# Kernel optimization log

Measured on AMD Instinct MI355X. Metric: run time of the kernel, lower is better.

The kernel has to match this reference:

```python
import jax, jax.numpy as jnp
import numpy as np

C_IN = 128
C_HID = 32
N_HEADS = 4
INF = 1000000000.0


def setup_inputs() -> dict:
    key = jax.random.key(0)
    ks = jax.random.split(key, 12)
    B, I, J = 1, 256, 256
    hc = N_HEADS * C_HID
    s = 0.02
    return {
        "x": jax.random.normal(ks[0], (B, I, J, C_IN), dtype=jnp.float32),
        "mask": jnp.ones((B, I, J), dtype=jnp.float32),
        "ln_w": jnp.ones((C_IN,), dtype=jnp.float32),
        "ln_b": jnp.zeros((C_IN,), dtype=jnp.float32),
        "w_tri": jax.random.normal(ks[1], (C_IN, N_HEADS), dtype=jnp.float32) * s,
        "wq": jax.random.normal(ks[2], (C_IN, hc), dtype=jnp.float32) * s,
        "wk": jax.random.normal(ks[3], (C_IN, hc), dtype=jnp.float32) * s,
        "wv": jax.random.normal(ks[4], (C_IN, hc), dtype=jnp.float32) * s,
        "wg": jax.random.normal(ks[5], (C_IN, hc), dtype=jnp.float32) * s,
        "bg": jnp.ones((hc,), dtype=jnp.float32),
        "wo": jax.random.normal(ks[6], (hc, C_IN), dtype=jnp.float32) * s,
        "bo": jnp.zeros((C_IN,), dtype=jnp.float32),
    }


def _layer_norm(x, w, b, eps=1e-5):
    mu = jnp.mean(x, axis=-1, keepdims=True)
    var = jnp.var(x, axis=-1, keepdims=True)
    return (x - mu) * jax.lax.rsqrt(var + eps) * w + b


def _triangle_attention(x, mask, ln_w, ln_b, w_tri, wq, wk, wv, wg, bg, wo, bo):
    # starting=True: no transpose. x: [B, I, J, C]
    B, I, J, C = x.shape
    x = _layer_norm(x, ln_w, ln_b)
    # mask_bias: [B, I, 1, 1, J]
    mask_bias = (INF * (mask - 1.0))[..., :, None, None, :]
    # triangle_bias: linear(x) -> [B, I, J, H], permute (2,0,1) -> [B, H, I, J], unsqueeze -> [B, 1, H, I, J]
    tri = jnp.einsum("bijc,ch->bhij", x, w_tri)[:, None]  # [B, 1, H, I, J]
    # q/k/v: [B, I, H, J, Ch]
    def proj(w):
        return jnp.einsum("bijc,c(" + "" + ")->bijc", x, w) if False else (
            (x @ w).reshape(B, I, J, N_HEADS, C_HID).transpose(0, 1, 3, 2, 4))
    q = proj(wq) * (C_HID ** -0.5)
    k = proj(wk)
    v = proj(wv)
    # scores: [B, I, H, J, J]; biases broadcast over H (mask_bias) / I (tri over b,1 dim matches i? no)
    scores = jnp.einsum("bihqc,bihkc->bihqk", q, k)
    scores = scores + mask_bias + tri  # tri [B,1,H,I,J] broadcasts: i-dim aligns with query? matches torch broadcast [B,I,H,J,J]+[B,1,H,J,J]... wait tri is [B,1,H,I,J] with I==J so it broadcasts over the batch-of-rows dim
    a = jax.nn.softmax(scores, axis=-1)
    o = jnp.einsum("bihqk,bihkc->bihqc", a, v)  # [B, I, H, J, Ch]
    o = o.transpose(0, 1, 3, 2, 4).reshape(B, I, J, N_HEADS * C_HID)
    g = jax.nn.sigmoid(x @ wg + bg)
    o = o * g
    return o @ wo + bo  # [B, I, J, C]


def reference(x, mask, ln_w, ln_b, w_tri, wq, wk, wv, wg, bg, wo, bo):
    return _triangle_attention(x, mask, ln_w, ln_b, w_tri, wq, wk, wv, wg, bg, wo, bo)
```

## Files before the change

### kernel.cpp

```cpp
#include <hip/hip_runtime.h>


typedef __attribute__((ext_vector_type(4))) float f32x4;
typedef __attribute__((ext_vector_type(8))) short bf16x8;
#define MFMA16(a, b, c) __builtin_amdgcn_mfma_f32_16x16x32_bf16(a, b, c, 0, 0, 0)
#define LOG2E 1.4426950408889634f

__device__ __forceinline__ float bf2f(unsigned int u16) {
    return __uint_as_float(u16 << 16);
}
__device__ __forceinline__ unsigned int f2bf(float f) {
    unsigned int u = __float_as_uint(f);
    return (u + 0x7fffu + ((u >> 16) & 1u)) >> 16;
}
__device__ __forceinline__ unsigned int pack2(float a, float b) {
    return f2bf(a) | (f2bf(b) << 16);
}
__device__ __forceinline__ unsigned int cvt_pk_bf16(float lo, float hi) {
    unsigned int r;
    asm("v_cvt_pk_bf16_f32 %0, %1, %2" : "=v"(r) : "v"(lo), "v"(hi));
    return r;
}

__global__ __launch_bounds__(128) void k_prep(
    const float* __restrict__ wq, const float* __restrict__ wk,
    const float* __restrict__ wv, const float* __restrict__ wg,
    const float* __restrict__ wo, unsigned short* __restrict__ wT)
{
    const int mat = blockIdx.x, k0 = blockIdx.y * 16, t = threadIdx.x;
    const float* W = (mat == 0) ? wq : (mat == 1) ? wk : (mat == 2) ? wv
                     : (mat == 3) ? wg : wo;
    unsigned short* T = wT + mat * 16384;
    float col[16];
    #pragma unroll
    for (int kk = 0; kk < 16; ++kk) col[kk] = W[(k0 + kk) * 128 + t];
    unsigned int pk[8];
    #pragma unroll
    for (int u = 0; u < 8; ++u) pk[u] = pack2(col[2 * u], col[2 * u + 1]);
    *(uint4*)(T + t * 128 + k0)     = make_uint4(pk[0], pk[1], pk[2], pk[3]);
    *(uint4*)(T + t * 128 + k0 + 8) = make_uint4(pk[4], pk[5], pk[6], pk[7]);
}

__global__ __launch_bounds__(256, 2) void k_lnproj(
    const float* __restrict__ x, const float* __restrict__ ln_w,
    const float* __restrict__ ln_b, const float* __restrict__ w_tri,
    const unsigned short* __restrict__ wT, const float* __restrict__ bg,
    unsigned short* __restrict__ qb, unsigned short* __restrict__ kb,
    unsigned short* __restrict__ vtb, unsigned short* __restrict__ gb,
    float* __restrict__ triT)
{
    __shared__ unsigned short sA[128 * 136];
    __shared__ unsigned short sB[128 * 136];
    __shared__ unsigned short sWt[16 * 136];

    const int t = threadIdx.x, w = t >> 6, lane = t & 63;
    const int l15 = lane & 15, g = lane >> 4;
    const int rowBase = blockIdx.x * 128;

    if (t < 128) {
        const float4 wv = ((const float4*)w_tri)[t];
        sWt[0 * 136 + t] = (unsigned short)f2bf(wv.x);
        sWt[1 * 136 + t] = (unsigned short)f2bf(wv.y);
        sWt[2 * 136 + t] = (unsigned short)f2bf(wv.z);
        sWt[3 * 136 + t] = (unsigned short)f2bf(wv.w);
    } else {
        #pragma unroll
        for (int u = 0; u < 13; ++u) {
            const int idx = (t - 128) + 128 * u;
            if (idx < 12 * 136) sWt[4 * 136 + idx] = 0;
        }
    }

    {
        const int r = t >> 1, half = t & 1;
        const float* xr = x + (size_t)(rowBase + r) * 128 + half * 64;
        float v[64];
        float s1 = 0.0f, s2 = 0.0f;
        #pragma unroll
        for (int u = 0; u < 16; ++u) {
            const float4 q4 = ((const float4*)xr)[u];
            v[4*u] = q4.x; v[4*u+1] = q4.y; v[4*u+2] = q4.z; v[4*u+3] = q4.w;
            s1 += q4.x + q4.y + q4.z + q4.w;
            s2 += q4.x*q4.x + q4.y*q4.y + q4.z*q4.z + q4.w*q4.w;
        }
        s1 += __shfl_xor(s1, 1);
        s2 += __shfl_xor(s2, 1);
        const float mu = s1 * (1.0f / 128.0f);
        const float rs = rsqrtf(s2 * (1.0f / 128.0f) - mu * mu + 1e-5f);
        const float4* lw = (const float4*)(ln_w + half * 64);
        const float4* lb = (const float4*)(ln_b + half * 64);
        #pragma unroll
        for (int u = 0; u < 16; ++u) {
            const float4 w4 = lw[u], b4 = lb[u];
            v[4*u]   = (v[4*u]   - mu) * rs * w4.x + b4.x;
            v[4*u+1] = (v[4*u+1] - mu) * rs * w4.y + b4.y;
            v[4*u+2] = (v[4*u+2] - mu) * rs * w4.z + b4.z;
            v[4*u+3] = (v[4*u+3] - mu) * rs * w4.w + b4.w;
        }
        #pragma unroll
        for (int u = 0; u < 8; ++u) {
            uint4 pk;
            pk.x = pack2(v[8*u],   v[8*u+1]);
            pk.y = pack2(v[8*u+2], v[8*u+3]);
            pk.z = pack2(v[8*u+4], v[8*u+5]);
            pk.w = pack2(v[8*u+6], v[8*u+7]);
            *(uint4*)&sA[r * 136 + half * 64 + u * 8] = pk;
        }
    }
    __syncthreads();

    bf16x8 af[2][4];
    #pragma unroll
    for (int m = 0; m < 2; ++m)
        #pragma unroll
        for (int ks = 0; ks < 4; ++ks)
            af[m][ks] = *(const bf16x8*)&sA[(w * 32 + m * 16 + l15) * 136 + ks * 32 + g * 8];

    #pragma unroll
    for (int m = 0; m < 2; ++m) {
        f32x4 tc = (f32x4){0.f, 0.f, 0.f, 0.f};
        #pragma unroll
        for (int ks = 0; ks < 4; ++ks) {
            const bf16x8 bfw = *(const bf16x8*)&sWt[l15 * 136 + ks * 32 + g * 8];
            tc = MFMA16(af[m][ks], bfw, tc);
        }
        if (l15 < 4) {
            #pragma unroll
            for (int reg = 0; reg < 4; ++reg) {
                const int gr = rowBase + w * 32 + m * 16 + 4 * g + reg;
                triT[l15 * 65536 + gr] = tc[reg] * LOG2E;
            }
        }
    }

    const int r2 = t >> 1, half2 = t & 1;
    for (int mat = 0; mat < 4; ++mat) {
        {
            const unsigned short* Wm = wT + mat * 16384 + r2 * 128 + half2 * 64;
            #pragma unroll
            for (int u = 0; u < 8; ++u)
                *(uint4*)&sB[r2 * 136 + half2 * 64 + u * 8] = *(const uint4*)(Wm + u * 8);
        }
        __syncthreads();

        f32x4 acc[2][8];
        #pragma unroll
        for (int m = 0; m < 2; ++m)
            #pragma unroll
            for (int n = 0; n < 8; ++n) acc[m][n] = (f32x4){0.f, 0.f, 0.f, 0.f};
        #pragma unroll
        for (int n = 0; n < 8; ++n)
            #pragma unroll
            for (int ks = 0; ks < 4; ++ks) {
                const bf16x8 bf = *(const bf16x8*)&sB[(n * 16 + l15) * 136 + ks * 32 + g * 8];
                acc[0][n] = MFMA16(af[0][ks], bf, acc[0][n]);
                acc[1][n] = MFMA16(af[1][ks], bf, acc[1][n]);
            }
        __syncthreads();

        float bgv[8];
        if (mat == 3) {
            #pragma unroll
            for (int n = 0; n < 8; ++n) bgv[n] = bg[n * 16 + l15];
        }
        const float scl = (mat == 0) ? 0.25503486245f : 1.0f;
        #pragma unroll
        for (int m = 0; m < 2; ++m)
            #pragma unroll
            for (int n = 0; n < 8; ++n) {
                float vv[4];
                #pragma unroll
                for (int reg = 0; reg < 4; ++reg) {
                    float z = acc[m][n][reg];
                    if (mat == 3) z = 1.0f / (1.0f + __expf(-(z + bgv[n])));
                    else z *= scl;
                    vv[reg] = z;
                }
                const unsigned int a01 = cvt_pk_bf16(vv[0], vv[1]);
                const unsigned int a23 = cvt_pk_bf16(vv[2], vv[3]);
                const int qr = w * 32 + m * 16 + g * 4;
                const int col = n * 16 + l15;
                sB[qr * 136 + col]       = (unsigned short)a01;
                sB[(qr + 1) * 136 + col] = (unsigned short)(a01 >> 16);
                sB[(qr + 2) * 136 + col] = (unsigned short)a23;
                sB[(qr + 3) * 136 + col] = (unsigned short)(a23 >> 16);
            }
        __syncthreads();

        const int row = rowBase + r2;
        if (mat < 2) {
            unsigned short* dst = (mat == 0) ? qb : kb;
            const int i = row >> 8, j = row & 255;
            #pragma unroll
            for (int u = 0; u < 8; ++u) {
                const int c0 = half2 * 64 + u * 8;
                const int hh = c0 >> 5, ch = c0 & 31;
                *(uint4*)(dst + (((size_t)(i * 4 + hh)) * 256 + j) * 32 + ch) =
                    *(const uint4*)&sB[r2 * 136 + c0];
            }
        } else if (mat == 2) {
            const int c = t & 127, jh = t >> 7;
            const int i = rowBase >> 8;
            const int j0 = (rowBase & 255) + jh * 64;
            unsigned short buf[64];
            #pragma unroll
            for (int u = 0; u < 64; ++u) buf[u] = sB[(jh * 64 + u) * 136 + c];
            unsigned short* dst = vtb + ((size_t)(i * 128 + c)) * 256 + j0;
            #pragma unroll
            for (int u = 0; u < 8; ++u)
                *(uint4*)(dst + u * 8) = *(uint4*)&buf[u * 8];
        } else {
            #pragma unroll
            for (int u = 0; u < 8; ++u) {
                const int c0 = half2 * 64 + u * 8;
                *(uint4*)(gb + (size_t)row * 128 + c0) = *(const uint4*)&sB[r2 * 136 + c0];
            }
        }
        __syncthreads();
    }
}

__global__ __launch_bounds__(256, 3) void k_attn6(
    const unsigned short* __restrict__ qb, const unsigned short* __restrict__ kb,
    const unsigned short* __restrict__ vtb, const float* __restrict__ mask,
    const float* __restrict__ triT, const unsigned short* __restrict__ gb,
    unsigned short* __restrict__ ob)
{
    __shared__ unsigned short sK[256 * 32];
    __shared__ unsigned short sVt[32 * 260];
    __shared__ unsigned short sP[4][64 * 36];
    __shared__ float sM[256];

    const int i = blockIdx.x, h = blockIdx.y, t = threadIdx.x;
    const int w = t >> 6, lane = t & 63, l15 = lane & 15, g = lane >> 4;
    const size_t base = (size_t)(i * 4 + h) * 8192;

    {
        const uint4* ks = (const uint4*)(kb + base + t * 32);
        char* kdst = (char*)sK + t * 64;
        const int kswz = (t & 3) << 4;
        #pragma unroll
        for (int u = 0; u < 4; ++u)
            *(uint4*)(kdst + ((u * 16) ^ kswz)) = ks[u];

        const int ch = t >> 3, seg = t & 7;
        const uint4* vs = (const uint4*)(vtb + base + (size_t)ch * 256 + seg * 32);
        unsigned short* vdst = &sVt[ch * 260 + seg * 32];
        #pragma unroll
        for (int u = 0; u < 4; ++u)
            *(uint4*)(vdst + u * 8) = vs[u];

        sM[t] = (LOG2E * 1.0e9f) * (mask[i * 256 + t] - 1.0f);
    }

    const int q0 = w * 64;
    bf16x8 qf[4];
    #pragma unroll
    for (int m = 0; m < 4; ++m)
        qf[m] = *(const bf16x8*)(qb + base + (size_t)(q0 + m * 16 + l15) * 32 + g * 8);

    bf16x8 ones;
    #pragma unroll
    for (int u = 0; u < 8; ++u) ones[u] = (short)0x3F80;

    __syncthreads();

    f32x4 acc[4][2], accL[4];
    #pragma unroll
    for (int m = 0; m < 4; ++m) {
        acc[m][0] = (f32x4){0.f, 0.f, 0.f, 0.f};
        acc[m][1] = (f32x4){0.f, 0.f, 0.f, 0.f};
        accL[m]   = (f32x4){0.f, 0.f, 0.f, 0.f};
    }

    unsigned short* sPw = &sP[w][0];
    const float* triQ = triT + h * 65536;
    const f32x4 zero = (f32x4){0.f, 0.f, 0.f, 0.f};

    #pragma unroll
    for (int kt = 0; kt < 4; ++kt) {
        const int kv0 = kt * 64;
        #pragma unroll
        for (int hh = 0; hh < 2; ++hh) {
            const int kvh = kv0 + hh * 32;

            bf16x8 kf[2];
            #pragma unroll
            for (int n2 = 0; n2 < 2; ++n2) {
                const int row = kvh + n2 * 16 + l15;
                kf[n2] = *(const bf16x8*)((const char*)sK + row * 64 +
                                          ((g * 16) ^ ((row & 3) << 4)));
            }
            float4 mk[2];
            #pragma unroll
            for (int n2 = 0; n2 < 2; ++n2)
                mk[n2] = *(const float4*)&sM[kvh + n2 * 16 + g * 4];

            float4 tvb[2][2];
            #pragma unroll
            for (int n2 = 0; n2 < 2; ++n2)
                tvb[0][n2] = *(const float4*)
                    (triQ + (q0 + l15) * 256 + kvh + n2 * 16 + g * 4);

            #pragma unroll
            for (int m = 0; m < 4; ++m) {
                f32x4 p[2];
                #pragma unroll
                for (int n2 = 0; n2 < 2; ++n2)
                    p[n2] = MFMA16(kf[n2], qf[m], zero);
                if (m < 3) {
                    #pragma unroll
                    for (int n2 = 0; n2 < 2; ++n2)
                        tvb[(m + 1) & 1][n2] = *(const float4*)
                            (triQ + (q0 + (m + 1) * 16 + l15) * 256 + kvh + n2 * 16 + g * 4);
                }
                #pragma unroll
                for (int n2 = 0; n2 < 2; ++n2) {
                    const float4 tv = tvb[m & 1][n2];
                    p[n2][0] = exp2f(p[n2][0] + mk[n2].x + tv.x);
                    p[n2][1] = exp2f(p[n2][1] + mk[n2].y + tv.y);
                    p[n2][2] = exp2f(p[n2][2] + mk[n2].z + tv.z);
                    p[n2][3] = exp2f(p[n2][3] + mk[n2].w + tv.w);
                }
                #pragma unroll
                for (int n2 = 0; n2 < 2; ++n2) {
                    const unsigned int a01 = cvt_pk_bf16(p[n2][0], p[n2][1]);
                    const unsigned int a23 = cvt_pk_bf16(p[n2][2], p[n2][3]);
                    *(uint2*)&sPw[(m * 16 + l15) * 36 + n2 * 16 + g * 4] =
                        make_uint2(a01, a23);
                }
            }

            const bf16x8 vf0 = *(const bf16x8*)&sVt[l15 * 260 + kvh + g * 8];
            const bf16x8 vf1 = *(const bf16x8*)&sVt[(16 + l15) * 260 + kvh + g * 8];
            #pragma unroll
            for (int m = 0; m < 4; ++m) {
                const bf16x8 pb = *(const bf16x8*)&sPw[(m * 16 + l15) * 36 + g * 8];
                acc[m][0] = MFMA16(vf0, pb, acc[m][0]);
                acc[m][1] = MFMA16(vf1, pb, acc[m][1]);
                accL[m]   = MFMA16(ones, pb, accL[m]);
            }
        }
    }

    #pragma unroll
    for (int m = 0; m < 4; ++m) {
        const float inv = 1.0f / accL[m][0];
        const int q = q0 + m * 16 + l15;
        const unsigned short* gp = gb + (size_t)(i * 256 + q) * 128 + h * 32;
        unsigned short* op = ob + (((size_t)(i * 256 + q)) * 4 + h) * 32;
        #pragma unroll
        for (int n2 = 0; n2 < 2; ++n2) {
            const uint2 gv = *(const uint2*)(gp + n2 * 16 + g * 4);
            const float g0 = bf2f(gv.x & 0xffffu), g1 = bf2f(gv.x >> 16);
            const float g2 = bf2f(gv.y & 0xffffu), g3 = bf2f(gv.y >> 16);
            const unsigned int a01 =
                cvt_pk_bf16(acc[m][n2][0] * inv * g0, acc[m][n2][1] * inv * g1);
            const unsigned int a23 =
                cvt_pk_bf16(acc[m][n2][2] * inv * g2, acc[m][n2][3] * inv * g3);
            *(uint2*)(op + n2 * 16 + g * 4) = make_uint2(a01, a23);
        }
    }
}

__global__ __launch_bounds__(256, 3) void k_out3(
    const unsigned short* __restrict__ ob, const unsigned short* __restrict__ woT,
    const float* __restrict__ bo, float* __restrict__ out)
{
    __shared__ unsigned short sA[128 * 136];
    __shared__ unsigned short sB[128 * 72];
    const int t = threadIdx.x, w = t >> 6, lane = t & 63;
    const int l15 = lane & 15, g = lane >> 4;
    const int rowBase = blockIdx.x * 128;
    const int r = t >> 1, half = t & 1;

    #pragma unroll
    for (int u = 0; u < 8; ++u) {
        const int c = half * 64 + u * 8;
        *(uint4*)&sA[r * 136 + c] = *(const uint4*)(ob + (size_t)(rowBase + r) * 128 + c);
    }

    f32x4 acc[2][8];
    #pragma unroll
    for (int m = 0; m < 2; ++m)
        #pragma unroll
        for (int n = 0; n < 8; ++n) acc[m][n] = (f32x4){0.f, 0.f, 0.f, 0.f};

    #pragma unroll
    for (int kc = 0; kc < 2; ++kc) {
        #pragma unroll
        for (int u = 0; u < 4; ++u)
            *(uint4*)&sB[r * 72 + half * 32 + u * 8] =
                *(const uint4*)(woT + r * 128 + kc * 64 + half * 32 + u * 8);
        __syncthreads();
        #pragma unroll
        for (int ks = 0; ks < 2; ++ks) {
            const bf16x8 a0 = *(const bf16x8*)
                &sA[(w * 32 + l15) * 136 + kc * 64 + ks * 32 + g * 8];
            const bf16x8 a1 = *(const bf16x8*)
                &sA[(w * 32 + 16 + l15) * 136 + kc * 64 + ks * 32 + g * 8];
            #pragma unroll
            for (int n = 0; n < 8; ++n) {
                const bf16x8 bf = *(const bf16x8*)&sB[(n * 16 + l15) * 72 + ks * 32 + g * 8];
                acc[0][n] = MFMA16(a0, bf, acc[0][n]);
                acc[1][n] = MFMA16(a1, bf, acc[1][n]);
            }
        }
        __syncthreads();
    }

    float bov[8];
    #pragma unroll
    for (int n = 0; n < 8; ++n) bov[n] = bo[n * 16 + l15];
    #pragma unroll
    for (int m = 0; m < 2; ++m)
        #pragma unroll
        for (int n = 0; n < 8; ++n)
            #pragma unroll
            for (int reg = 0; reg < 4; ++reg) {
                const int row = rowBase + w * 32 + m * 16 + g * 4 + reg;
                out[(size_t)row * 128 + n * 16 + l15] = acc[m][n][reg] + bov[n];
            }
}

extern "C" void kernel_launch(void* const* d_in, const int* in_sizes, int n_in,
                              void* d_out, int out_size, void* d_ws, size_t ws_size,
                              hipStream_t stream) {
    (void)in_sizes; (void)n_in; (void)out_size; (void)ws_size;
    const float* x     = (const float*)d_in[0];
    const float* mask  = (const float*)d_in[1];
    const float* ln_w  = (const float*)d_in[2];
    const float* ln_b  = (const float*)d_in[3];
    const float* w_tri = (const float*)d_in[4];
    const float* wq    = (const float*)d_in[5];
    const float* wk    = (const float*)d_in[6];
    const float* wv    = (const float*)d_in[7];
    const float* wg    = (const float*)d_in[8];
    const float* bg    = (const float*)d_in[9];
    const float* wo    = (const float*)d_in[10];
    const float* bo    = (const float*)d_in[11];
    float* out = (float*)d_out;

    char* ws = (char*)d_ws;
    unsigned short* qb   = (unsigned short*)(ws + (16u << 20));
    unsigned short* kb   = (unsigned short*)(ws + (32u << 20));
    unsigned short* vtb  = (unsigned short*)(ws + (48u << 20));
    unsigned short* gb   = (unsigned short*)(ws + (64u << 20));
    unsigned short* ob   = (unsigned short*)(ws + (80u << 20));
    float*          triT = (float*)(ws + (96u << 20));
    unsigned short* wT   = (unsigned short*)(ws + (97u << 20));

    k_prep<<<dim3(5, 8), 128, 0, stream>>>(wq, wk, wv, wg, wo, wT);
    k_lnproj<<<512, 256, 0, stream>>>(x, ln_w, ln_b, w_tri, wT, bg,
                                      qb, kb, vtb, gb, triT);
    k_attn6<<<dim3(256, 4), 256, 0, stream>>>(qb, kb, vtb, mask, triT, gb, ob);
    k_out3<<<512, 256, 0, stream>>>(ob, wT + 4 * 16384, bo, out);
}
```

Baseline: 106.3 us.

## Shrink projection tiles, stage weights via registers, bf16 triangle bias, V from global

The LN+projection kernel now processes 64 rows per block instead of 128, with smaller LDS buffers and a register-prefetched, K-chunked weight staging pipeline, targeting higher occupancy. The triangle-bias weights are transposed once in the prep kernel. The triangle bias is stored in bf16 instead of fp32, halving its traffic in attention. The attention kernel drops the V shared-memory tile and loads V fragments straight from global into registers, freeing LDS for four blocks per CU. The cost is extra global reads of V and weights, plus reduced bias precision.

```diff
diff --git a/kernel.cpp b/kernel.cpp
--- a/kernel.cpp
+++ b/kernel.cpp
@@ -25,9 +25,23 @@
 __global__ __launch_bounds__(128) void k_prep(
     const float* __restrict__ wq, const float* __restrict__ wk,
     const float* __restrict__ wv, const float* __restrict__ wg,
-    const float* __restrict__ wo, unsigned short* __restrict__ wT)
+    const float* __restrict__ wo, const float* __restrict__ w_tri,
+    unsigned short* __restrict__ wT, unsigned short* __restrict__ wtT)
 {
-    const int mat = blockIdx.x, k0 = blockIdx.y * 16, t = threadIdx.x;
+    const int mat = blockIdx.x, t = threadIdx.x;
+    if (mat == 5) {
+        if (blockIdx.y == 0) {
+            const float4 wv4 = ((const float4*)w_tri)[t];
+            wtT[0 * 128 + t] = (unsigned short)f2bf(wv4.x);
+            wtT[1 * 128 + t] = (unsigned short)f2bf(wv4.y);
+            wtT[2 * 128 + t] = (unsigned short)f2bf(wv4.z);
+            wtT[3 * 128 + t] = (unsigned short)f2bf(wv4.w);
+            #pragma unroll
+            for (int n = 4; n < 16; ++n) wtT[n * 128 + t] = 0;
+        }
+        return;
+    }
+    const int k0 = blockIdx.y * 16;
     const float* W = (mat == 0) ? wq : (mat == 1) ? wk : (mat == 2) ? wv
                      : (mat == 3) ? wg : wo;
     unsigned short* T = wT + mat * 16384;
@@ -41,56 +55,42 @@
     *(uint4*)(T + t * 128 + k0 + 8) = make_uint4(pk[4], pk[5], pk[6], pk[7]);
 }
 
-__global__ __launch_bounds__(256, 2) void k_lnproj(
+__global__ __launch_bounds__(256, 4) void k_lnproj(
     const float* __restrict__ x, const float* __restrict__ ln_w,
-    const float* __restrict__ ln_b, const float* __restrict__ w_tri,
+    const float* __restrict__ ln_b, const unsigned short* __restrict__ wtT,
     const unsigned short* __restrict__ wT, const float* __restrict__ bg,
     unsigned short* __restrict__ qb, unsigned short* __restrict__ kb,
     unsigned short* __restrict__ vtb, unsigned short* __restrict__ gb,
-    float* __restrict__ triT)
+    unsigned short* __restrict__ triTb)
 {
-    __shared__ unsigned short sA[128 * 136];
-    __shared__ unsigned short sB[128 * 136];
-    __shared__ unsigned short sWt[16 * 136];
+    __shared__ unsigned short sA[64 * 136];
+    __shared__ unsigned short sB[128 * 72];
 
     const int t = threadIdx.x, w = t >> 6, lane = t & 63;
     const int l15 = lane & 15, g = lane >> 4;
-    const int rowBase = blockIdx.x * 128;
-
-    if (t < 128) {
-        const float4 wv = ((const float4*)w_tri)[t];
-        sWt[0 * 136 + t] = (unsigned short)f2bf(wv.x);
-        sWt[1 * 136 + t] = (unsigned short)f2bf(wv.y);
-        sWt[2 * 136 + t] = (unsigned short)f2bf(wv.z);
-        sWt[3 * 136 + t] = (unsigned short)f2bf(wv.w);
-    } else {
-        #pragma unroll
-        for (int u = 0; u < 13; ++u) {
-            const int idx = (t - 128) + 128 * u;
-            if (idx < 12 * 136) sWt[4 * 136 + idx] = 0;
-        }
-    }
+    const int rowBase = blockIdx.x * 64;
+    const int i_ = rowBase >> 8, j0 = rowBase & 255;
 
     {
-        const int r = t >> 1, half = t & 1;
-        const float* xr = x + (size_t)(rowBase + r) * 128 + half * 64;
-        float v[64];
+        const int r = t >> 2, qd = t & 3;
+        const float* xr = x + (size_t)(rowBase + r) * 128 + qd * 32;
+        float v[32];
         float s1 = 0.0f, s2 = 0.0f;
         #pragma unroll
-        for (int u = 0; u < 16; ++u) {
+        for (int u = 0; u < 8; ++u) {
             const float4 q4 = ((const float4*)xr)[u];
             v[4*u] = q4.x; v[4*u+1] = q4.y; v[4*u+2] = q4.z; v[4*u+3] = q4.w;
             s1 += q4.x + q4.y + q4.z + q4.w;
             s2 += q4.x*q4.x + q4.y*q4.y + q4.z*q4.z + q4.w*q4.w;
         }
-        s1 += __shfl_xor(s1, 1);
-        s2 += __shfl_xor(s2, 1);
+        s1 += __shfl_xor(s1, 1); s1 += __shfl_xor(s1, 2);
+        s2 += __shfl_xor(s2, 1); s2 += __shfl_xor(s2, 2);
         const float mu = s1 * (1.0f / 128.0f);
         const float rs = rsqrtf(s2 * (1.0f / 128.0f) - mu * mu + 1e-5f);
-        const float4* lw = (const float4*)(ln_w + half * 64);
-        const float4* lb = (const float4*)(ln_b + half * 64);
-        #pragma unroll
-        for (int u = 0; u < 16; ++u) {
+        const float4* lw = (const float4*)(ln_w + qd * 32);
+        const float4* lb = (const float4*)(ln_b + qd * 32);
+        #pragma unroll
+        for (int u = 0; u < 8; ++u) {
             const float4 w4 = lw[u], b4 = lb[u];
             v[4*u]   = (v[4*u]   - mu) * rs * w4.x + b4.x;
             v[4*u+1] = (v[4*u+1] - mu) * rs * w4.y + b4.y;
@@ -98,64 +98,75 @@
             v[4*u+3] = (v[4*u+3] - mu) * rs * w4.w + b4.w;
         }
         #pragma unroll
-        for (int u = 0; u < 8; ++u) {
+        for (int u = 0; u < 4; ++u) {
             uint4 pk;
             pk.x = pack2(v[8*u],   v[8*u+1]);
             pk.y = pack2(v[8*u+2], v[8*u+3]);
             pk.z = pack2(v[8*u+4], v[8*u+5]);
             pk.w = pack2(v[8*u+6], v[8*u+7]);
-            *(uint4*)&sA[r * 136 + half * 64 + u * 8] = pk;
+            *(uint4*)&sA[(t >> 2) * 136 + qd * 32 + u * 8] = pk;
         }
     }
     __syncthreads();
 
-    bf16x8 af[2][4];
-    #pragma unroll
-    for (int m = 0; m < 2; ++m)
-        #pragma unroll
-        for (int ks = 0; ks < 4; ++ks)
-            af[m][ks] = *(const bf16x8*)&sA[(w * 32 + m * 16 + l15) * 136 + ks * 32 + g * 8];
-
-    #pragma unroll
-    for (int m = 0; m < 2; ++m) {
+    {
         f32x4 tc = (f32x4){0.f, 0.f, 0.f, 0.f};
         #pragma unroll
         for (int ks = 0; ks < 4; ++ks) {
-            const bf16x8 bfw = *(const bf16x8*)&sWt[l15 * 136 + ks * 32 + g * 8];
-            tc = MFMA16(af[m][ks], bfw, tc);
+            const bf16x8 afr = *(const bf16x8*)&sA[(w * 16 + l15) * 136 + ks * 32 + g * 8];
+            const bf16x8 bfw = *(const bf16x8*)(wtT + l15 * 128 + ks * 32 + g * 8);
+            tc = MFMA16(afr, bfw, tc);
         }
         if (l15 < 4) {
             #pragma unroll
             for (int reg = 0; reg < 4; ++reg) {
-                const int gr = rowBase + w * 32 + m * 16 + 4 * g + reg;
-                triT[l15 * 65536 + gr] = tc[reg] * LOG2E;
-            }
-        }
-    }
-
-    const int r2 = t >> 1, half2 = t & 1;
+                const int gr = rowBase + w * 16 + 4 * g + reg;
+                triTb[l15 * 65536 + gr] = (unsigned short)f2bf(tc[reg] * LOG2E);
+            }
+        }
+    }
+
+    const int wr = t >> 1, wh = t & 1;
+    uint4 wreg[4];
+    {
+        const unsigned short* p = wT + wr * 128 + wh * 32;
+        #pragma unroll
+        for (int u = 0; u < 4; ++u) wreg[u] = *(const uint4*)(p + u * 8);
+    }
+
     for (int mat = 0; mat < 4; ++mat) {
-        {
-            const unsigned short* Wm = wT + mat * 16384 + r2 * 128 + half2 * 64;
-            #pragma unroll
-            for (int u = 0; u < 8; ++u)
-                *(uint4*)&sB[r2 * 136 + half2 * 64 + u * 8] = *(const uint4*)(Wm + u * 8);
-        }
-        __syncthreads();
-
-        f32x4 acc[2][8];
-        #pragma unroll
-        for (int m = 0; m < 2; ++m)
-            #pragma unroll
-            for (int n = 0; n < 8; ++n) acc[m][n] = (f32x4){0.f, 0.f, 0.f, 0.f};
-        #pragma unroll
-        for (int n = 0; n < 8; ++n)
-            #pragma unroll
-            for (int ks = 0; ks < 4; ++ks) {
-                const bf16x8 bf = *(const bf16x8*)&sB[(n * 16 + l15) * 136 + ks * 32 + g * 8];
-                acc[0][n] = MFMA16(af[0][ks], bf, acc[0][n]);
-                acc[1][n] = MFMA16(af[1][ks], bf, acc[1][n]);
-            }
+        f32x4 acc[8];
+        #pragma unroll
+        for (int n = 0; n < 8; ++n) acc[n] = (f32x4){0.f, 0.f, 0.f, 0.f};
+
+        #pragma unroll
+        for (int kc = 0; kc < 2; ++kc) {
+            __syncthreads();
+            #pragma unroll
+            for (int u = 0; u < 4; ++u)
+                *(uint4*)&sB[wr * 72 + wh * 32 + u * 8] = wreg[u];
+            const int s = mat * 2 + kc;
+            if (s < 7) {
+                const int nm = (s + 1) >> 1, nk = (s + 1) & 1;
+                const unsigned short* p = wT + nm * 16384 + wr * 128 + nk * 64 + wh * 32;
+                #pragma unroll
+                for (int u = 0; u < 4; ++u) wreg[u] = *(const uint4*)(p + u * 8);
+            }
+            __syncthreads();
+
+            bf16x8 afc[2];
+            #pragma unroll
+            for (int ks = 0; ks < 2; ++ks)
+                afc[ks] = *(const bf16x8*)
+                    &sA[(w * 16 + l15) * 136 + kc * 64 + ks * 32 + g * 8];
+            #pragma unroll
+            for (int n = 0; n < 8; ++n)
+                #pragma unroll
+                for (int ks = 0; ks < 2; ++ks) {
+                    const bf16x8 bf = *(const bf16x8*)&sB[(n * 16 + l15) * 72 + ks * 32 + g * 8];
+                    acc[n] = MFMA16(afc[ks], bf, acc[n]);
+                }
+        }
         __syncthreads();
 
         float bgv[8];
@@ -165,69 +176,64 @@
         }
         const float scl = (mat == 0) ? 0.25503486245f : 1.0f;
         #pragma unroll
-        for (int m = 0; m < 2; ++m)
-            #pragma unroll
-            for (int n = 0; n < 8; ++n) {
-                float vv[4];
-                #pragma unroll
-                for (int reg = 0; reg < 4; ++reg) {
-                    float z = acc[m][n][reg];
-                    if (mat == 3) z = 1.0f / (1.0f + __expf(-(z + bgv[n])));
-                    else z *= scl;
-                    vv[reg] = z;
-                }
-                const unsigned int a01 = cvt_pk_bf16(vv[0], vv[1]);
-                const unsigned int a23 = cvt_pk_bf16(vv[2], vv[3]);
-                const int qr = w * 32 + m * 16 + g * 4;
-                const int col = n * 16 + l15;
-                sB[qr * 136 + col]       = (unsigned short)a01;
-                sB[(qr + 1) * 136 + col] = (unsigned short)(a01 >> 16);
-                sB[(qr + 2) * 136 + col] = (unsigned short)a23;
-                sB[(qr + 3) * 136 + col] = (unsigned short)(a23 >> 16);
-            }
+        for (int n = 0; n < 8; ++n) {
+            float vv[4];
+            #pragma unroll
+            for (int reg = 0; reg < 4; ++reg) {
+                float z = acc[n][reg];
+                if (mat == 3) z = 1.0f / (1.0f + __expf(-(z + bgv[n])));
+                else z *= scl;
+                vv[reg] = z;
+            }
+            const unsigned int a01 = cvt_pk_bf16(vv[0], vv[1]);
+            const unsigned int a23 = cvt_pk_bf16(vv[2], vv[3]);
+            const int qr = w * 16 + g * 4;
+            const int col = n * 16 + l15;
+            sB[qr * 136 + col]       = (unsigned short)a01;
+            sB[(qr + 1) * 136 + col] = (unsigned short)(a01 >> 16);
+            sB[(qr + 2) * 136 + col] = (unsigned short)a23;
+            sB[(qr + 3) * 136 + col] = (unsigned short)(a23 >> 16);
+        }
         __syncthreads();
 
-        const int row = rowBase + r2;
         if (mat < 2) {
             unsigned short* dst = (mat == 0) ? qb : kb;
-            const int i = row >> 8, j = row & 255;
-            #pragma unroll
-            for (int u = 0; u < 8; ++u) {
-                const int c0 = half2 * 64 + u * 8;
-                const int hh = c0 >> 5, ch = c0 & 31;
-                *(uint4*)(dst + (((size_t)(i * 4 + hh)) * 256 + j) * 32 + ch) =
-                    *(const uint4*)&sB[r2 * 136 + c0];
+            #pragma unroll
+            for (int rr = 0; rr < 4; ++rr) {
+                const int r2 = rr * 16 + (lane >> 2);
+                const int j = j0 + r2, ch = (lane & 3) * 8;
+                *(uint4*)(dst + (((size_t)(i_ * 4 + w)) * 256 + j) * 32 + ch) =
+                    *(const uint4*)&sB[r2 * 136 + w * 32 + ch];
             }
         } else if (mat == 2) {
-            const int c = t & 127, jh = t >> 7;
-            const int i = rowBase >> 8;
-            const int j0 = (rowBase & 255) + jh * 64;
-            unsigned short buf[64];
-            #pragma unroll
-            for (int u = 0; u < 64; ++u) buf[u] = sB[(jh * 64 + u) * 136 + c];
-            unsigned short* dst = vtb + ((size_t)(i * 128 + c)) * 256 + j0;
-            #pragma unroll
-            for (int u = 0; u < 8; ++u)
-                *(uint4*)(dst + u * 8) = *(uint4*)&buf[u * 8];
+            const int hc = w * 32 + (lane >> 1);
+            const int joff = (lane & 1) * 32;
+            unsigned short* dst = vtb + ((size_t)(i_ * 128 + hc)) * 256 + j0 + joff;
+            #pragma unroll
+            for (int u = 0; u < 4; ++u) {
+                unsigned short buf[8];
+                #pragma unroll
+                for (int k = 0; k < 8; ++k)
+                    buf[k] = sB[(joff + u * 8 + k) * 136 + hc];
+                *(uint4*)(dst + u * 8) = *(uint4*)&buf[0];
+            }
         } else {
-            #pragma unroll
-            for (int u = 0; u < 8; ++u) {
-                const int c0 = half2 * 64 + u * 8;
-                *(uint4*)(gb + (size_t)row * 128 + c0) = *(const uint4*)&sB[r2 * 136 + c0];
-            }
-        }
-        __syncthreads();
-    }
-}
-
-__global__ __launch_bounds__(256, 3) void k_attn6(
+            const int r2 = t >> 2, qd = t & 3;
+            #pragma unroll
+            for (int u = 0; u < 4; ++u)
+                *(uint4*)(gb + (size_t)(rowBase + r2) * 128 + qd * 32 + u * 8) =
+                    *(const uint4*)&sB[r2 * 136 + qd * 32 + u * 8];
+        }
+    }
+}
+
+__global__ __launch_bounds__(256, 4) void k_attn7(
     const unsigned short* __restrict__ qb, const unsigned short* __restrict__ kb,
     const unsigned short* __restrict__ vtb, const float* __restrict__ mask,
-    const float* __restrict__ triT, const unsigned short* __restrict__ gb,
+    const unsigned short* __restrict__ triTb, const unsigned short* __restrict__ gb,
     unsigned short* __restrict__ ob)
 {
     __shared__ unsigned short sK[256 * 32];
-    __shared__ unsigned short sVt[32 * 260];
     __shared__ unsigned short sP[4][64 * 36];
     __shared__ float sM[256];
 
@@ -242,14 +248,6 @@
         #pragma unroll
         for (int u = 0; u < 4; ++u)
             *(uint4*)(kdst + ((u * 16) ^ kswz)) = ks[u];
-
-        const int ch = t >> 3, seg = t & 7;
-        const uint4* vs = (const uint4*)(vtb + base + (size_t)ch * 256 + seg * 32);
-        unsigned short* vdst = &sVt[ch * 260 + seg * 32];
-        #pragma unroll
-        for (int u = 0; u < 4; ++u)
-            *(uint4*)(vdst + u * 8) = vs[u];
-
         sM[t] = (LOG2E * 1.0e9f) * (mask[i * 256 + t] - 1.0f);
     }
 
@@ -274,12 +272,20 @@
     }
 
     unsigned short* sPw = &sP[w][0];
-    const float* triQ = triT + h * 65536;
+    const unsigned short* triQ = triTb + h * 65536;
+    const unsigned short* vbase = vtb + base;
     const f32x4 zero = (f32x4){0.f, 0.f, 0.f, 0.f};
 
     #pragma unroll
     for (int kt = 0; kt < 4; ++kt) {
         const int kv0 = kt * 64;
+        bf16x8 vreg[4];
+        #pragma unroll
+        for (int hh = 0; hh < 2; ++hh) {
+            vreg[hh * 2]     = *(const bf16x8*)(vbase + (size_t)l15 * 256 + kv0 + hh * 32 + g * 8);
+            vreg[hh * 2 + 1] = *(const bf16x8*)(vbase + (size_t)(16 + l15) * 256 + kv0 + hh * 32 + g * 8);
+        }
+
         #pragma unroll
         for (int hh = 0; hh < 2; ++hh) {
             const int kvh = kv0 + hh * 32;
@@ -296,10 +302,10 @@
             for (int n2 = 0; n2 < 2; ++n2)
                 mk[n2] = *(const float4*)&sM[kvh + n2 * 16 + g * 4];
 
-            float4 tvb[2][2];
+            ushort4 tvb[2][2];
             #pragma unroll
             for (int n2 = 0; n2 < 2; ++n2)
-                tvb[0][n2] = *(const float4*)
+                tvb[0][n2] = *(const ushort4*)
                     (triQ + (q0 + l15) * 256 + kvh + n2 * 16 + g * 4);
 
             #pragma unroll
@@ -311,16 +317,16 @@
                 if (m < 3) {
                     #pragma unroll
                     for (int n2 = 0; n2 < 2; ++n2)
-                        tvb[(m + 1) & 1][n2] = *(const float4*)
+                        tvb[(m + 1) & 1][n2] = *(const ushort4*)
                             (triQ + (q0 + (m + 1) * 16 + l15) * 256 + kvh + n2 * 16 + g * 4);
                 }
                 #pragma unroll
                 for (int n2 = 0; n2 < 2; ++n2) {
-                    const float4 tv = tvb[m & 1][n2];
-                    p[n2][0] = exp2f(p[n2][0] + mk[n2].x + tv.x);
-                    p[n2][1] = exp2f(p[n2][1] + mk[n2].y + tv.y);
-                    p[n2][2] = exp2f(p[n2][2] + mk[n2].z + tv.z);
-                    p[n2][3] = exp2f(p[n2][3] + mk[n2].w + tv.w);
+                    const ushort4 tv = tvb[m & 1][n2];
+                    p[n2][0] = exp2f(p[n2][0] + mk[n2].x + bf2f(tv.x));
+                    p[n2][1] = exp2f(p[n2][1] + mk[n2].y + bf2f(tv.y));
+                    p[n2][2] = exp2f(p[n2][2] + mk[n2].z + bf2f(tv.z));
+                    p[n2][3] = exp2f(p[n2][3] + mk[n2].w + bf2f(tv.w));
                 }
                 #pragma unroll
                 for (int n2 = 0; n2 < 2; ++n2) {
@@ -331,8 +337,8 @@
                 }
             }
 
-            const bf16x8 vf0 = *(const bf16x8*)&sVt[l15 * 260 + kvh + g * 8];
-            const bf16x8 vf1 = *(const bf16x8*)&sVt[(16 + l15) * 260 + kvh + g * 8];
+            const bf16x8 vf0 = vreg[hh * 2];
+            const bf16x8 vf1 = vreg[hh * 2 + 1];
             #pragma unroll
             for (int m = 0; m < 4; ++m) {
                 const bf16x8 pb = *(const bf16x8*)&sPw[(m * 16 + l15) * 36 + g * 8];
@@ -442,17 +448,18 @@
     float* out = (float*)d_out;
 
     char* ws = (char*)d_ws;
-    unsigned short* qb   = (unsigned short*)(ws + (16u << 20));
-    unsigned short* kb   = (unsigned short*)(ws + (32u << 20));
-    unsigned short* vtb  = (unsigned short*)(ws + (48u << 20));
-    unsigned short* gb   = (unsigned short*)(ws + (64u << 20));
-    unsigned short* ob   = (unsigned short*)(ws + (80u << 20));
-    float*          triT = (float*)(ws + (96u << 20));
-    unsigned short* wT   = (unsigned short*)(ws + (97u << 20));
-
-    k_prep<<<dim3(5, 8), 128, 0, stream>>>(wq, wk, wv, wg, wo, wT);
-    k_lnproj<<<512, 256, 0, stream>>>(x, ln_w, ln_b, w_tri, wT, bg,
-                                      qb, kb, vtb, gb, triT);
-    k_attn6<<<dim3(256, 4), 256, 0, stream>>>(qb, kb, vtb, mask, triT, gb, ob);
+    unsigned short* qb    = (unsigned short*)(ws + (16u << 20));
+    unsigned short* kb    = (unsigned short*)(ws + (32u << 20));
+    unsigned short* vtb   = (unsigned short*)(ws + (48u << 20));
+    unsigned short* gb    = (unsigned short*)(ws + (64u << 20));
+    unsigned short* ob    = (unsigned short*)(ws + (80u << 20));
+    unsigned short* triTb = (unsigned short*)(ws + (96u << 20));
+    unsigned short* wT    = (unsigned short*)(ws + (97u << 20));
+    unsigned short* wtT   = (unsigned short*)(ws + (97u << 20) + 163840);
+
+    k_prep<<<dim3(6, 8), 128, 0, stream>>>(wq, wk, wv, wg, wo, w_tri, wT, wtT);
+    k_lnproj<<<1024, 256, 0, stream>>>(x, ln_w, ln_b, wtT, wT, bg,
+                                       qb, kb, vtb, gb, triTb);
+    k_attn7<<<dim3(256, 4), 256, 0, stream>>>(qb, kb, vtb, mask, triTb, gb, ob);
     k_out3<<<512, 256, 0, stream>>>(ob, wT + 4 * 16384, bo, out);
 }
```

Result: slower. 129.0 us (+21.3%).
